# Kernel optimization log

Measured on AMD Instinct MI355X. Metric: run time of the kernel, lower is better.

The kernel has to match this reference:

```python
import jax, jax.numpy as jnp
import numpy as np

EMP = 0.1       # threshold from init
EPS = 1e-8      # torch.cosine_similarity eps
ZERO = 9e-15    # replacement value below threshold


def setup_inputs() -> dict:
    key = jax.random.key(0)
    k1, k2 = jax.random.split(key)
    B, N, F = 4, 4096, 64
    x = jax.random.normal(k1, (B, N, F), dtype=jnp.float32)
    w = jax.random.normal(k2, (1, N, F), dtype=jnp.float32)
    return {"x": x, "w": w}


def reference(x, w):
    # x: (B, N, F); w: (1, N, F)
    xw = x * w
    # cosine similarity via normalize + matmul (torch eps clamp on norms)
    nrm = jnp.maximum(jnp.sqrt(jnp.sum(xw * xw, axis=-1, keepdims=True)), EPS)
    xn = xw / nrm                                  # (B, N, F)
    cos = jnp.einsum('bif,bjf->bij', xn, xn)       # (B, N, N)
    return jnp.where(cos > EMP, cos, jnp.asarray(ZERO, cos.dtype))
```

## Files before the change

### kernel.cpp

```cpp
#include <hip/hip_runtime.h>
#include <hip/hip_bf16.h>

typedef _Float16 f16x8 __attribute__((ext_vector_type(8)));
typedef float f32x4 __attribute__((ext_vector_type(4)));

#define N_ROWS 4096
#define F_DIM 64
#define BATCH 4
#define EMPF 0.1f
#define EMPD 0.1
#define ZEROV 9e-15f
#define WINDOW 2e-4f
#define REG_CAP 256u
#define N_BLOCKS 4096

__global__ __launch_bounds__(256) void normalize_split_kernel(
    const float* __restrict__ x, const float* __restrict__ w,
    _Float16* __restrict__ hi, _Float16* __restrict__ lo) {
  const int lane = threadIdx.x & 63;
  const int wid = threadIdx.x >> 6;
  const int rg = blockIdx.x * 4 + wid;
  const int n = rg & (N_ROWS - 1);
  const float xv = x[rg * F_DIM + lane];
  const float wv = w[n * F_DIM + lane];
  const float p = xv * wv;
  float s = p * p;
#pragma unroll
  for (int off = 32; off >= 1; off >>= 1) s += __shfl_xor(s, off, 64);
  const float nrm = fmaxf(sqrtf(s), 1e-8f);
  const float xn = p / nrm;
  const _Float16 h = (_Float16)xn;
  const float rem = xn - (float)h;
  hi[rg * F_DIM + lane] = h;
  lo[rg * F_DIM + lane] = (_Float16)rem;
}

__global__ __launch_bounds__(256) void gram_kernel(
    const _Float16* __restrict__ hi, const _Float16* __restrict__ lo,
    float* __restrict__ out, unsigned* __restrict__ cnt,
    unsigned* __restrict__ regions) {
  __shared__ unsigned lds_cnt;
  if (threadIdx.x == 0) lds_cnt = 0;
  __syncthreads();

  const int lane = threadIdx.x & 63;
  const int wid = threadIdx.x >> 6;
  const int wm = wid >> 1, wn = wid & 1;
  const int b = blockIdx.z;
  const int row0 = blockIdx.x * 128 + wm * 64;
  const int col0 = blockIdx.y * 128 + wn * 64;
  const int rbase = b * N_ROWS;
  const unsigned bid =
      ((unsigned)blockIdx.z * gridDim.y + blockIdx.y) * gridDim.x + blockIdx.x;
  unsigned* __restrict__ region = regions + (size_t)bid * REG_CAP;

  const int lr = lane & 15;
  const int lk = (lane >> 4) * 8;

  f16x8 ah[2][4], al[2][4];
#pragma unroll
  for (int kf = 0; kf < 2; ++kf)
#pragma unroll
    for (int i = 0; i < 4; ++i) {
      const int ra = (rbase + row0 + i * 16 + lr) * F_DIM + kf * 32 + lk;
      ah[kf][i] = *(const f16x8*)(hi + ra);
      al[kf][i] = *(const f16x8*)(lo + ra);
    }

  const int r_in = lane & 15;
  const int cb = (lane >> 4) * 4;

#pragma unroll 1
  for (int j = 0; j < 4; ++j) {
    f16x8 bh[2], bl[2];
#pragma unroll
    for (int kf = 0; kf < 2; ++kf) {
      const int rb = (rbase + col0 + j * 16 + lr) * F_DIM + kf * 32 + lk;
      bh[kf] = *(const f16x8*)(hi + rb);
      bl[kf] = *(const f16x8*)(lo + rb);
    }
    f32x4 acc[4] = {};
#pragma unroll
    for (int i = 0; i < 4; ++i) {
#pragma unroll
      for (int kf = 0; kf < 2; ++kf) {
        acc[i] = __builtin_amdgcn_mfma_f32_16x16x32_f16(bh[kf], ah[kf][i], acc[i], 0, 0, 0);
        acc[i] = __builtin_amdgcn_mfma_f32_16x16x32_f16(bh[kf], al[kf][i], acc[i], 0, 0, 0);
        acc[i] = __builtin_amdgcn_mfma_f32_16x16x32_f16(bl[kf], ah[kf][i], acc[i], 0, 0, 0);
      }
    }
#pragma unroll
    for (int i = 0; i < 4; ++i) {
      f32x4 v = acc[i];
      const int row = row0 + i * 16 + r_in;
      const int col = col0 + j * 16 + cb;
      const bool near = fabsf(v[0] - EMPF) < WINDOW || fabsf(v[1] - EMPF) < WINDOW ||
                        fabsf(v[2] - EMPF) < WINDOW || fabsf(v[3] - EMPF) < WINDOW;
      if (__builtin_expect(__any((int)near), 0)) {
#pragma unroll
        for (int r = 0; r < 4; ++r) {
          if (fabsf(v[r] - EMPF) < WINDOW) {
            const unsigned pos = atomicAdd(&lds_cnt, 1u);
            if (pos < REG_CAP)
              region[pos] = ((unsigned)b << 24) | ((unsigned)row << 12) | (unsigned)(col + r);
          }
        }
      }
#pragma unroll
      for (int r = 0; r < 4; ++r) v[r] = (v[r] > EMPF) ? v[r] : ZEROV;
      const size_t oi = ((size_t)b << 24) + ((size_t)row << 12) + (size_t)col;
      *(f32x4*)(out + oi) = v;
    }
  }

  __syncthreads();
  if (threadIdx.x == 0) cnt[bid] = lds_cnt < REG_CAP ? lds_cnt : REG_CAP;
}

__global__ __launch_bounds__(256) void refine_kernel(
    const float* __restrict__ x, const float* __restrict__ w,
    float* __restrict__ out, const unsigned* __restrict__ cnt,
    const unsigned* __restrict__ regions) {
  const int lane = threadIdx.x & 63;
  const unsigned wg0 = blockIdx.x * (blockDim.x >> 6) + (threadIdx.x >> 6);
  const unsigned nw = gridDim.x * (blockDim.x >> 6);
  for (unsigned rgn = wg0; rgn < N_BLOCKS; rgn += nw) {
    const unsigned count = cnt[rgn];
    const unsigned* __restrict__ region = regions + (size_t)rgn * REG_CAP;
    for (unsigned e = 0; e < count; ++e) {
      const unsigned ent = region[e];
      const int b = (int)(ent >> 24);
      const int i = (int)((ent >> 12) & 4095);
      const int j = (int)(ent & 4095);
      const double wi = (double)w[i * F_DIM + lane];
      const double wj = (double)w[j * F_DIM + lane];
      const double xi = (double)x[(b * N_ROWS + i) * F_DIM + lane];
      const double xj = (double)x[(b * N_ROWS + j) * F_DIM + lane];
      const double pi = xi * wi;
      const double pj = xj * wj;
      double si = pi * pi, sj = pj * pj, sij = pi * pj;
#pragma unroll
      for (int off = 32; off >= 1; off >>= 1) {
        si += __shfl_xor(si, off, 64);
        sj += __shfl_xor(sj, off, 64);
        sij += __shfl_xor(sij, off, 64);
      }
      if (lane == 0) {
        const double ni = fmax(sqrt(si), 1e-8);
        const double nj = fmax(sqrt(sj), 1e-8);
        const double c = sij / (ni * nj);
        const double res = (c > EMPD) ? c : (double)ZEROV;
        out[((size_t)b << 24) + ((size_t)i << 12) + (size_t)j] = (float)res;
      }
    }
  }
}

extern "C" void kernel_launch(void* const* d_in, const int* in_sizes, int n_in,
                              void* d_out, int out_size, void* d_ws, size_t ws_size,
                              hipStream_t stream) {
  const float* x = (const float*)d_in[0];
  const float* w = (const float*)d_in[1];
  float* out = (float*)d_out;

  char* ws = (char*)d_ws;
  _Float16* hi = (_Float16*)ws;
  _Float16* lo = (_Float16*)(ws + (size_t)16384 * 64 * 2);
  unsigned* cnt = (unsigned*)(ws + (size_t)4 * 1024 * 1024);
  unsigned* regions = (unsigned*)(ws + (size_t)4 * 1024 * 1024 + 16384);

  normalize_split_kernel<<<4096, 256, 0, stream>>>(x, w, hi, lo);
  gram_kernel<<<dim3(32, 32, 4), 256, 0, stream>>>(hi, lo, out, cnt, regions);
  refine_kernel<<<1024, 256, 0, stream>>>(x, w, out, cnt, regions);
}
```

Baseline: 130.7 us.

## Reshape gram tiling into per-wave long column strips with B-fragment prefetch

Changes the gram kernel from 128x128 block tiles with 4 waves to 512-thread blocks where each wave owns a 32-row by 512-column strip. It loops over 32 column tiles and software-prefetches the next B fragments from global memory. Near-threshold bookkeeping moves to per-wave LDS counters and regions, so the block-wide barriers go away. The aim is fewer block launches, better A-fragment reuse and overlapped loads, at the cost of fewer rows per tile and different store locality.

```diff
diff --git a/kernel.cpp b/kernel.cpp
--- a/kernel.cpp
+++ b/kernel.cpp
@@ -6,13 +6,12 @@
 
 #define N_ROWS 4096
 #define F_DIM 64
-#define BATCH 4
 #define EMPF 0.1f
 #define EMPD 0.1
 #define ZEROV 9e-15f
 #define WINDOW 2e-4f
 #define REG_CAP 256u
-#define N_BLOCKS 4096
+#define N_REGIONS 4096
 
 __global__ __launch_bounds__(256) void normalize_split_kernel(
     const float* __restrict__ x, const float* __restrict__ w,
@@ -35,72 +34,75 @@
   lo[rg * F_DIM + lane] = (_Float16)rem;
 }
 
-__global__ __launch_bounds__(256) void gram_kernel(
+__global__ __launch_bounds__(512, 4) void gram_kernel(
     const _Float16* __restrict__ hi, const _Float16* __restrict__ lo,
     float* __restrict__ out, unsigned* __restrict__ cnt,
     unsigned* __restrict__ regions) {
-  __shared__ unsigned lds_cnt;
-  if (threadIdx.x == 0) lds_cnt = 0;
-  __syncthreads();
-
+  __shared__ unsigned lds_cnt[8];
   const int lane = threadIdx.x & 63;
   const int wid = threadIdx.x >> 6;
-  const int wm = wid >> 1, wn = wid & 1;
-  const int b = blockIdx.z;
-  const int row0 = blockIdx.x * 128 + wm * 64;
-  const int col0 = blockIdx.y * 128 + wn * 64;
+  if (lane == 0) lds_cnt[wid] = 0;
+
+  const int b = blockIdx.y;
+  const int row0 = blockIdx.x * 32;
   const int rbase = b * N_ROWS;
-  const unsigned bid =
-      ((unsigned)blockIdx.z * gridDim.y + blockIdx.y) * gridDim.x + blockIdx.x;
-  unsigned* __restrict__ region = regions + (size_t)bid * REG_CAP;
+  const unsigned rgn = (((unsigned)b * gridDim.x + blockIdx.x) << 3) | (unsigned)wid;
+  unsigned* __restrict__ region = regions + (size_t)rgn * REG_CAP;
 
   const int lr = lane & 15;
   const int lk = (lane >> 4) * 8;
 
-  f16x8 ah[2][4], al[2][4];
+  f16x8 ah[2][2], al[2][2];
 #pragma unroll
-  for (int kf = 0; kf < 2; ++kf)
+  for (int g = 0; g < 2; ++g)
 #pragma unroll
-    for (int i = 0; i < 4; ++i) {
-      const int ra = (rbase + row0 + i * 16 + lr) * F_DIM + kf * 32 + lk;
-      ah[kf][i] = *(const f16x8*)(hi + ra);
-      al[kf][i] = *(const f16x8*)(lo + ra);
+    for (int kf = 0; kf < 2; ++kf) {
+      const int ra = (rbase + row0 + g * 16 + lr) * F_DIM + kf * 32 + lk;
+      ah[g][kf] = *(const f16x8*)(hi + ra);
+      al[g][kf] = *(const f16x8*)(lo + ra);
     }
 
   const int r_in = lane & 15;
   const int cb = (lane >> 4) * 4;
+  const int colbase = wid * 512;
+
+  int rb = (rbase + colbase + lr) * F_DIM + lk;
+  f16x8 bh0 = *(const f16x8*)(hi + rb);
+  f16x8 bl0 = *(const f16x8*)(lo + rb);
+  f16x8 bh1 = *(const f16x8*)(hi + rb + 32);
+  f16x8 bl1 = *(const f16x8*)(lo + rb + 32);
 
 #pragma unroll 1
-  for (int j = 0; j < 4; ++j) {
-    f16x8 bh[2], bl[2];
+  for (int j = 0; j < 32; ++j) {
+    const int rbn = rb + (j < 31 ? 16 * F_DIM : 0);
+    f16x8 nbh0 = *(const f16x8*)(hi + rbn);
+    f16x8 nbl0 = *(const f16x8*)(lo + rbn);
+    f16x8 nbh1 = *(const f16x8*)(hi + rbn + 32);
+    f16x8 nbl1 = *(const f16x8*)(lo + rbn + 32);
+
+    f32x4 acc[2] = {};
 #pragma unroll
-    for (int kf = 0; kf < 2; ++kf) {
-      const int rb = (rbase + col0 + j * 16 + lr) * F_DIM + kf * 32 + lk;
-      bh[kf] = *(const f16x8*)(hi + rb);
-      bl[kf] = *(const f16x8*)(lo + rb);
+    for (int g = 0; g < 2; ++g) {
+      acc[g] = __builtin_amdgcn_mfma_f32_16x16x32_f16(bh0, ah[g][0], acc[g], 0, 0, 0);
+      acc[g] = __builtin_amdgcn_mfma_f32_16x16x32_f16(bh0, al[g][0], acc[g], 0, 0, 0);
+      acc[g] = __builtin_amdgcn_mfma_f32_16x16x32_f16(bl0, ah[g][0], acc[g], 0, 0, 0);
+      acc[g] = __builtin_amdgcn_mfma_f32_16x16x32_f16(bh1, ah[g][1], acc[g], 0, 0, 0);
+      acc[g] = __builtin_amdgcn_mfma_f32_16x16x32_f16(bh1, al[g][1], acc[g], 0, 0, 0);
+      acc[g] = __builtin_amdgcn_mfma_f32_16x16x32_f16(bl1, ah[g][1], acc[g], 0, 0, 0);
     }
-    f32x4 acc[4] = {};
+
+    const int col = colbase + j * 16 + cb;
 #pragma unroll
-    for (int i = 0; i < 4; ++i) {
-#pragma unroll
-      for (int kf = 0; kf < 2; ++kf) {
-        acc[i] = __builtin_amdgcn_mfma_f32_16x16x32_f16(bh[kf], ah[kf][i], acc[i], 0, 0, 0);
-        acc[i] = __builtin_amdgcn_mfma_f32_16x16x32_f16(bh[kf], al[kf][i], acc[i], 0, 0, 0);
-        acc[i] = __builtin_amdgcn_mfma_f32_16x16x32_f16(bl[kf], ah[kf][i], acc[i], 0, 0, 0);
-      }
-    }
-#pragma unroll
-    for (int i = 0; i < 4; ++i) {
-      f32x4 v = acc[i];
-      const int row = row0 + i * 16 + r_in;
-      const int col = col0 + j * 16 + cb;
+    for (int g = 0; g < 2; ++g) {
+      f32x4 v = acc[g];
+      const int row = row0 + g * 16 + r_in;
       const bool near = fabsf(v[0] - EMPF) < WINDOW || fabsf(v[1] - EMPF) < WINDOW ||
                         fabsf(v[2] - EMPF) < WINDOW || fabsf(v[3] - EMPF) < WINDOW;
       if (__builtin_expect(__any((int)near), 0)) {
 #pragma unroll
         for (int r = 0; r < 4; ++r) {
           if (fabsf(v[r] - EMPF) < WINDOW) {
-            const unsigned pos = atomicAdd(&lds_cnt, 1u);
+            const unsigned pos = atomicAdd(&lds_cnt[wid], 1u);
             if (pos < REG_CAP)
               region[pos] = ((unsigned)b << 24) | ((unsigned)row << 12) | (unsigned)(col + r);
           }
@@ -111,10 +113,15 @@
       const size_t oi = ((size_t)b << 24) + ((size_t)row << 12) + (size_t)col;
       *(f32x4*)(out + oi) = v;
     }
+
+    bh0 = nbh0; bl0 = nbl0; bh1 = nbh1; bl1 = nbl1;
+    rb += 16 * F_DIM;
   }
 
-  __syncthreads();
-  if (threadIdx.x == 0) cnt[bid] = lds_cnt < REG_CAP ? lds_cnt : REG_CAP;
+  if (lane == 0) {
+    const unsigned c = lds_cnt[wid];
+    cnt[rgn] = c < REG_CAP ? c : REG_CAP;
+  }
 }
 
 __global__ __launch_bounds__(256) void refine_kernel(
@@ -124,7 +131,7 @@
   const int lane = threadIdx.x & 63;
   const unsigned wg0 = blockIdx.x * (blockDim.x >> 6) + (threadIdx.x >> 6);
   const unsigned nw = gridDim.x * (blockDim.x >> 6);
-  for (unsigned rgn = wg0; rgn < N_BLOCKS; rgn += nw) {
+  for (unsigned rgn = wg0; rgn < N_REGIONS; rgn += nw) {
     const unsigned count = cnt[rgn];
     const unsigned* __restrict__ region = regions + (size_t)rgn * REG_CAP;
     for (unsigned e = 0; e < count; ++e) {
@@ -170,6 +177,6 @@
   unsigned* regions = (unsigned*)(ws + (size_t)4 * 1024 * 1024 + 16384);
 
   normalize_split_kernel<<<4096, 256, 0, stream>>>(x, w, hi, lo);
-  gram_kernel<<<dim3(32, 32, 4), 256, 0, stream>>>(hi, lo, out, cnt, regions);
+  gram_kernel<<<dim3(128, 4), 512, 0, stream>>>(hi, lo, out, cnt, regions);
   refine_kernel<<<1024, 256, 0, stream>>>(x, w, out, cnt, regions);
 }
```

New measurement: 138.6 us. +6.1%, slower.
